# Performance work log

Hardware: AMD Instinct MI355X
Metric: run time of the kernel (lower is better)

## Reference

```python
import jax, jax.numpy as jnp
import numpy as np

NUM_HEADS = 4
CATEGORY_SIZE = 128
DIM = 192
B, N, M = 2, 65000, 64


def setup_inputs() -> dict:
    key = jax.random.key(0)
    k1, k2, k3, k4 = jax.random.split(key, 4)
    qkv = jax.random.normal(k1, (B, N, 3 * DIM), dtype=jnp.float32)
    sim = jax.random.normal(k2, (B, N, M), dtype=jnp.float32)
    proj_w = jax.random.normal(k3, (DIM, DIM), dtype=jnp.float32) * (1.0 / np.sqrt(DIM))
    proj_b = jax.random.normal(k4, (DIM,), dtype=jnp.float32) * 0.01
    logit_scale = jnp.log(10.0 * jnp.ones((1, 1), dtype=jnp.float32))
    return {"qkv": qkv, "sim": sim, "proj_w": proj_w, "proj_b": proj_b,
            "logit_scale": logit_scale, "x_size": 65000}


def reference(qkv, sim, proj_w, proj_b, logit_scale, x_size):
    b, n, c3 = qkv.shape
    c = c3 // 3
    h = NUM_HEADS
    gs = min(n, CATEGORY_SIZE)
    ng = (n + gs - 1) // gs
    pad_n = ng * gs - n

    # token -> category id, then sort tokens by category
    tk_id = jnp.argmax(sim, axis=-1)                      # (b, n) int
    sort_idx = jnp.argsort(tk_id, axis=-1)                # (b, n)
    inv_idx = jnp.argsort(sort_idx, axis=-1)              # inverse permutation

    shuffled = jnp.take_along_axis(qkv, sort_idx[..., None], axis=1)  # (b, n, 3c)
    if pad_n > 0:
        pad = jnp.flip(shuffled[:, n - pad_n:n, :], axis=1)
        shuffled = jnp.concatenate([shuffled, pad], axis=1)           # (b, n+pad_n, 3c)

    # (3, b, ng, h, gs, c/h)
    y = shuffled.reshape(b, ng, gs, 3, h, c // h).transpose(3, 0, 1, 4, 2, 5)
    q, k, v = y[0], y[1], y[2]

    scale = jnp.exp(jnp.minimum(logit_scale, jnp.log(jnp.asarray(100.0, dtype=qkv.dtype))))
    attn = jnp.einsum('bghqd,bghkd->bghqk', q, k) * scale  # (b, ng, h, gs, gs)
    attn = jax.nn.softmax(attn, axis=-1)
    out = jnp.einsum('bghqk,bghkd->bghqd', attn, v)        # (b, ng, h, gs, c/h)
    out = out.transpose(0, 1, 3, 2, 4).reshape(b, n + pad_n, c)[:, :n, :]

    # scatter back to original token order
    out = jnp.take_along_axis(out, inv_idx[..., None], axis=1)
    return out @ proj_w.T + proj_b
```

## Files before the change

kernel.cpp:

```cpp
#include <hip/hip_runtime.h>
#include <hip/hip_bf16.h>
#include <math.h>

#define BB 2
#define NN 65000
#define MM 64
#define DIM 192
#define NH 4
#define HD 48
#define GS 128
#define NG 508
#define SORT_TPB 256
#define NBLK 254

#define XROWS 65024
#define XTILES_B 1016

typedef __attribute__((ext_vector_type(8))) short bf16x8;
typedef __attribute__((ext_vector_type(8))) _Float16 f16x8;
typedef __attribute__((ext_vector_type(2))) __fp16 fp16x2;
typedef __attribute__((ext_vector_type(4))) float f32x4;
typedef __attribute__((ext_vector_type(16))) float f32x16;
typedef __attribute__((ext_vector_type(8))) unsigned short u16x8;

__device__ __forceinline__ unsigned short f2bf(float f) {
  __hip_bfloat16 h = __float2bfloat16(f);
  return *(unsigned short*)&h;
}
__device__ __forceinline__ unsigned int pkh(float lo, float hi) {
  fp16x2 t = __builtin_amdgcn_cvt_pkrtz(lo, hi);
  return *(unsigned int*)&t;
}
__device__ __forceinline__ f16x8 cvt8h(float4 a, float4 b) {
  f16x8 r;
  r[0] = (_Float16)a.x; r[1] = (_Float16)a.y; r[2] = (_Float16)a.z; r[3] = (_Float16)a.w;
  r[4] = (_Float16)b.x; r[5] = (_Float16)b.y; r[6] = (_Float16)b.z; r[7] = (_Float16)b.w;
  return r;
}
__device__ __forceinline__ void gload_lds16(const float* src, float* lds_dst) {
  __builtin_amdgcn_global_load_lds(
      (const __attribute__((address_space(1))) unsigned int*)src,
      (__attribute__((address_space(3))) unsigned int*)lds_dst, 16, 0, 0);
}

__global__ void k_argmax_hist(const float* __restrict__ sim, int* __restrict__ tk,
                              int* __restrict__ hist) {
  __shared__ int cnt[MM];
  const int b = blockIdx.y, blk = blockIdx.x;
  if (threadIdx.x < MM) cnt[threadIdx.x] = 0;
  __syncthreads();
  int t = blk * SORT_TPB + threadIdx.x;
  if (t < NN) {
    const float4* row = (const float4*)(sim + ((size_t)b * NN + t) * MM);
    float best = -INFINITY;
    int bi = 0;
#pragma unroll
    for (int j = 0; j < MM / 4; ++j) {
      float4 v = row[j];
      if (v.x > best) { best = v.x; bi = 4 * j + 0; }
      if (v.y > best) { best = v.y; bi = 4 * j + 1; }
      if (v.z > best) { best = v.z; bi = 4 * j + 2; }
      if (v.w > best) { best = v.w; bi = 4 * j + 3; }
    }
    tk[b * NN + t] = bi;
    atomicAdd(&cnt[bi], 1);
  }
  __syncthreads();
  if (threadIdx.x < MM)
    hist[(b * NBLK + blk) * MM + threadIdx.x] = cnt[threadIdx.x];
}

#define SEGS 16
#define SEGB 16
__global__ void k_scan(const int* __restrict__ hist, int* __restrict__ boff) {
  const int b = blockIdx.x;
  const int tid = threadIdx.x;
  const int seg = tid >> 6, bin = tid & 63;
  __shared__ int part[SEGS][MM];
  __shared__ int basev[MM];
  const int lo = seg * SEGB;
  const int hi = min(NBLK, lo + SEGB);
  int s = 0;
  for (int blk = lo; blk < hi; ++blk) s += hist[(b * NBLK + blk) * MM + bin];
  part[seg][bin] = s;
  __syncthreads();
  if (tid < 64) {
    int tot = 0;
#pragma unroll
    for (int s2 = 0; s2 < SEGS; ++s2) tot += part[s2][bin];
    int incl = tot;
#pragma unroll
    for (int d = 1; d < 64; d <<= 1) {
      int o = __shfl_up(incl, d);
      if (bin >= d) incl += o;
    }
    basev[bin] = incl - tot;
  }
  __syncthreads();
  int run = basev[bin];
  for (int s2 = 0; s2 < seg; ++s2) run += part[s2][bin];
  for (int blk = lo; blk < hi; ++blk) {
    int h = hist[(b * NBLK + blk) * MM + bin];
    boff[(b * NBLK + blk) * MM + bin] = run;
    run += h;
  }
}

__global__ void k_scatter(const int* __restrict__ tk, const int* __restrict__ boff,
                          int* __restrict__ sidx) {
  __shared__ int whist[4][MM];
  const int b = blockIdx.y, blk = blockIdx.x;
  const int tid = threadIdx.x;
  const int w = tid >> 6, lane = tid & 63;
  ((int*)whist)[tid] = 0;
  __syncthreads();
  int t = blk * SORT_TPB + tid;
  int bin = (t < NN) ? tk[b * NN + t] : -1;
  unsigned long long m = ~0ull;
#pragma unroll
  for (int bit = 0; bit < 6; ++bit) {
    unsigned long long bl = __ballot((bin >> bit) & 1);
    m &= ((bin >> bit) & 1) ? bl : ~bl;
  }
  int rank_w = __popcll(m & ((1ull << lane) - 1ull));
  if (bin >= 0 && rank_w == 0) whist[w][bin] = __popcll(m);
  __syncthreads();
  if (bin >= 0) {
    int rank = rank_w;
#pragma unroll
    for (int w2 = 0; w2 < 3; ++w2)
      if (w2 < w) rank += whist[w2][bin];
    int pos = boff[(b * NBLK + blk) * MM + bin] + rank;
    sidx[b * NN + pos] = t;
  }
}

__global__ __launch_bounds__(256) void k_attn_mfma(const float* __restrict__ qkv,
                                                   const int* __restrict__ sidx,
                                                   const float* __restrict__ logit_scale,
                                                   __hip_bfloat16* __restrict__ attn_out) {
  const int x = blockIdx.x;
  const int g = ((x >> 5) << 3) + (x & 7);
  const int hd = (x >> 3) & 3;
  const int b = blockIdx.z;
  if (g >= NG) return;

  __shared__ int stok[GS];
  __shared__ __align__(16) _Float16 akv[4 * 3 * 64 * 8];
  __shared__ __align__(16) _Float16 vfrag[2 * 8 * 64 * 8];

  const int tid = threadIdx.x;
  const int w = tid >> 6, l = tid & 63;
  const int hl = l >> 5, l31 = l & 31;

  if (tid < GS) {
    int s = g * GS + tid;
    int sp = (s < NN) ? s : (2 * NN - 1 - s);
    stok[tid] = sidx[b * NN + sp];
  }
  __syncthreads();

#pragma unroll
  for (int i = 0; i < 3; ++i) {
    int c = tid + 256 * i;
    int ts = c >> 6, cl = c & 63;
    int kvr = (ts / 3) * 32 + (cl & 31);
    int dbase = (ts % 3) * 16 + (cl >> 5) * 8;
    const float* src = qkv + (size_t)(b * NN + stok[kvr]) * (3 * DIM) + DIM + hd * HD + dbase;
    ((f16x8*)akv)[c] = cvt8h(((const float4*)src)[0], ((const float4*)src)[1]);
  }

#pragma unroll
  for (int i = 0; i < 4; ++i) {
    int c = tid + 256 * i;
    int ntks = c >> 6, cl = c & 63;
    int nt = ntks >> 3, ks = ntks & 7;
    int d = nt * 32 + (cl & 31);
    int kvb = ks * 16 + (cl >> 5) * 8;
    _Float16 tmp[8];
    if (d < HD) {
#pragma unroll
      for (int e = 0; e < 8; ++e)
        tmp[e] = (_Float16)qkv[(size_t)(b * NN + stok[kvb + e]) * (3 * DIM) + 2 * DIM + hd * HD + d];
    } else {
#pragma unroll
      for (int e = 0; e < 8; ++e) tmp[e] = (_Float16)0.f;
    }
    ((f16x8*)vfrag)[c] = *(f16x8*)tmp;
  }

  f16x8 qf[3];
  {
    const float* qsrc = qkv + (size_t)(b * NN + stok[w * 32 + l31]) * (3 * DIM) + hd * HD;
#pragma unroll
    for (int s = 0; s < 3; ++s) {
      const float4* p = (const float4*)(qsrc + s * 16 + hl * 8);
      qf[s] = cvt8h(p[0], p[1]);
    }
  }
  __syncthreads();

  f32x16 accS[4];
#pragma unroll
  for (int t = 0; t < 4; ++t)
#pragma unroll
    for (int r = 0; r < 16; ++r) accS[t][r] = 0.f;

#pragma unroll
  for (int t = 0; t < 4; ++t)
#pragma unroll
    for (int s = 0; s < 3; ++s) {
      f16x8 af = ((const f16x8*)akv)[(t * 3 + s) * 64 + l];
      accS[t] = __builtin_amdgcn_mfma_f32_32x32x16_f16(af, qf[s], accS[t], 0, 0, 0);
    }

  const float scale = expf(fminf(logit_scale[0], 4.6051701860f));
  float mx = -INFINITY;
#pragma unroll
  for (int t = 0; t < 4; ++t)
#pragma unroll
    for (int r = 0; r < 16; ++r) { accS[t][r] *= scale; mx = fmaxf(mx, accS[t][r]); }
  mx = fmaxf(mx, __shfl_xor(mx, 32));
  float sum = 0.f;
#pragma unroll
  for (int t = 0; t < 4; ++t)
#pragma unroll
    for (int r = 0; r < 16; ++r) { float p = __expf(accS[t][r] - mx); accS[t][r] = p; sum += p; }
  sum += __shfl_xor(sum, 32);
  const float inv = 1.f / sum;
#pragma unroll
  for (int t = 0; t < 4; ++t)
#pragma unroll
    for (int r = 0; r < 16; ++r) accS[t][r] *= inv;

  f32x16 accO[2];
#pragma unroll
  for (int nt = 0; nt < 2; ++nt)
#pragma unroll
    for (int r = 0; r < 16; ++r) accO[nt][r] = 0.f;

#pragma unroll
  for (int t = 0; t < 4; ++t) {
    union { unsigned int u[4]; f16x8 v; } fa, fb;
    {
      unsigned int a0 = pkh(accS[t][0], accS[t][1]);
      unsigned int a1 = pkh(accS[t][2], accS[t][3]);
      unsigned int b0 = pkh(accS[t][4], accS[t][5]);
      unsigned int b1 = pkh(accS[t][6], accS[t][7]);
      unsigned int sa0 = __shfl_xor(a0, 32), sa1 = __shfl_xor(a1, 32);
      unsigned int sb0 = __shfl_xor(b0, 32), sb1 = __shfl_xor(b1, 32);
      fa.u[0] = hl ? sb0 : a0; fa.u[1] = hl ? sb1 : a1;
      fa.u[2] = hl ? b0 : sa0; fa.u[3] = hl ? b1 : sa1;
    }
    {
      unsigned int a0 = pkh(accS[t][8], accS[t][9]);
      unsigned int a1 = pkh(accS[t][10], accS[t][11]);
      unsigned int b0 = pkh(accS[t][12], accS[t][13]);
      unsigned int b1 = pkh(accS[t][14], accS[t][15]);
      unsigned int sa0 = __shfl_xor(a0, 32), sa1 = __shfl_xor(a1, 32);
      unsigned int sb0 = __shfl_xor(b0, 32), sb1 = __shfl_xor(b1, 32);
      fb.u[0] = hl ? sb0 : a0; fb.u[1] = hl ? sb1 : a1;
      fb.u[2] = hl ? b0 : sa0; fb.u[3] = hl ? b1 : sa1;
    }
    accO[0] = __builtin_amdgcn_mfma_f32_32x32x16_f16(fa.v, ((const f16x8*)vfrag)[(0 * 8 + 2 * t) * 64 + l], accO[0], 0, 0, 0);
    accO[1] = __builtin_amdgcn_mfma_f32_32x32x16_f16(fa.v, ((const f16x8*)vfrag)[(1 * 8 + 2 * t) * 64 + l], accO[1], 0, 0, 0);
    accO[0] = __builtin_amdgcn_mfma_f32_32x32x16_f16(fb.v, ((const f16x8*)vfrag)[(0 * 8 + 2 * t + 1) * 64 + l], accO[0], 0, 0, 0);
    accO[1] = __builtin_amdgcn_mfma_f32_32x32x16_f16(fb.v, ((const f16x8*)vfrag)[(1 * 8 + 2 * t + 1) * 64 + l], accO[1], 0, 0, 0);
  }

#pragma unroll
  for (int r = 0; r < 16; ++r) {
    int rowl = w * 32 + (r & 3) + 8 * (r >> 2) + 4 * hl;
    int sg = g * GS + rowl;
    if (sg < NN) {
      size_t base = ((size_t)b * XROWS + sg) * DIM + hd * HD;
      attn_out[base + l31] = __float2bfloat16(accO[0][r]);
      if (l31 < 16) attn_out[base + 32 + l31] = __float2bfloat16(accO[1][r]);
    }
  }
}

__global__ void k_wpack(const float* __restrict__ W, unsigned short* __restrict__ wpack) {
  int idx = blockIdx.x * blockDim.x + threadIdx.x;
  if (idx >= 12 * 6 * 64) return;
  int lane = idx & 63;
  int kkjt = idx >> 6;
  int kk = kkjt % 6;
  int jt = kkjt / 6;
  int j = jt * 16 + (lane & 15);
  int k0 = kk * 32 + (lane >> 4) * 8;
  const float* src = W + (size_t)j * DIM + k0;
  unsigned short tmp[8];
#pragma unroll
  for (int e = 0; e < 8; ++e) tmp[e] = f2bf(src[e]);
  ((u16x8*)wpack)[idx] = *(const u16x8*)tmp;
}

__global__ __launch_bounds__(256) void k_proj_mfma(const unsigned short* __restrict__ xb,
                                                   const int* __restrict__ sidx,
                                                   const unsigned short* __restrict__ wpack,
                                                   const float* __restrict__ bias,
                                                   float* __restrict__ out) {
  __shared__ unsigned short wl[12 * 6 * 64 * 8];
  const int tid = threadIdx.x;

#pragma unroll
  for (int j = 0; j < 18; ++j) {
    int c = j * 256 + tid;
    gload_lds16((const float*)((const u16x8*)wpack + c), (float*)((u16x8*)wl + c));
  }

  const int wid = tid >> 6, lane = tid & 63;
  const int l15 = lane & 15, lk = lane >> 4;

  float bv[12];
#pragma unroll
  for (int jt = 0; jt < 12; ++jt) bv[jt] = bias[jt * 16 + l15];

  __syncthreads();

  for (int tile = blockIdx.x; tile < BB * XTILES_B; tile += gridDim.x) {
    const int b = tile / XTILES_B;
    const int r0 = (tile % XTILES_B) * 64 + wid * 16;
    f32x4 acc[12];
#pragma unroll
    for (int jt = 0; jt < 12; ++jt) { f32x4 t = {bv[jt], bv[jt], bv[jt], bv[jt]}; acc[jt] = t; }

    const unsigned short* xrow = xb + ((size_t)b * XROWS + r0 + l15) * DIM;
#pragma unroll
    for (int kk = 0; kk < 6; ++kk) {
      bf16x8 a = *(const bf16x8*)(xrow + kk * 32 + lk * 8);
#pragma unroll
      for (int jt = 0; jt < 12; ++jt) {
        bf16x8 bfr = *(const bf16x8*)(wl + ((jt * 6 + kk) * 64 + lane) * 8);
        acc[jt] = __builtin_amdgcn_mfma_f32_16x16x32_bf16(a, bfr, acc[jt], 0, 0, 0);
      }
    }

    const int rowb = r0 + lk * 4;
    int orow[4];
#pragma unroll
    for (int r = 0; r < 4; ++r)
      orow[r] = (rowb + r < NN) ? sidx[b * NN + rowb + r] : -1;

#pragma unroll
    for (int jt = 0; jt < 12; ++jt) {
#pragma unroll
      for (int r = 0; r < 4; ++r) {
        if (orow[r] >= 0)
          out[((size_t)b * NN + orow[r]) * DIM + jt * 16 + l15] = acc[jt][r];
      }
    }
  }
}

extern "C" void kernel_launch(void* const* d_in, const int* in_sizes, int n_in,
                              void* d_out, int out_size, void* d_ws, size_t ws_size,
                              hipStream_t stream) {
  const float* qkv = (const float*)d_in[0];
  const float* sim = (const float*)d_in[1];
  const float* proj_w = (const float*)d_in[2];
  const float* proj_b = (const float*)d_in[3];
  const float* logit_scale = (const float*)d_in[4];

  unsigned short* x_bf16 = (unsigned short*)d_ws;
  unsigned short* wpack = x_bf16 + (size_t)BB * XROWS * DIM;
  int* tk = (int*)(wpack + 12 * 6 * 64 * 8);
  int* hist = tk + (size_t)BB * NN;
  int* boff = hist + (size_t)BB * NBLK * MM;
  int* sidx = boff + (size_t)BB * NBLK * MM;

  k_argmax_hist<<<dim3(NBLK, BB), SORT_TPB, 0, stream>>>(sim, tk, hist);
  k_scan<<<BB, 1024, 0, stream>>>(hist, boff);
  k_scatter<<<dim3(NBLK, BB), SORT_TPB, 0, stream>>>(tk, boff, sidx);
  k_wpack<<<(12 * 6 * 64 + 255) / 256, 256, 0, stream>>>(proj_w, wpack);
  k_attn_mfma<<<dim3(2048, 1, BB), 256, 0, stream>>>(qkv, sidx, logit_scale,
                                                     (__hip_bfloat16*)x_bf16);
  k_proj_mfma<<<dim3(1016), 256, 0, stream>>>(x_bf16, sidx, wpack, proj_b, (float*)d_out);
}
```

Baseline: 161.5 us.

## Process all four heads of a group in one 1024-thread attention block

The attention kernel now launches one 1024-thread block per group and batch, with each 256-thread slice handling one head, instead of one 256-thread block per (group, head). The sorted-token index load into shared memory happens once per group rather than once per head, and the padded grid entries with early return are gone. Shared memory per block grows fourfold, and 1024-thread blocks with heavy MFMA register use may cap occupancy or constrain register allocation under the larger launch bound.

```diff
diff --git a/kernel.cpp b/kernel.cpp
--- a/kernel.cpp
+++ b/kernel.cpp
@@ -135,22 +135,21 @@
   }
 }
 
-__global__ __launch_bounds__(256) void k_attn_mfma(const float* __restrict__ qkv,
-                                                   const int* __restrict__ sidx,
-                                                   const float* __restrict__ logit_scale,
-                                                   __hip_bfloat16* __restrict__ attn_out) {
-  const int x = blockIdx.x;
-  const int g = ((x >> 5) << 3) + (x & 7);
-  const int hd = (x >> 3) & 3;
+__global__ __launch_bounds__(1024) void k_attn_mfma(const float* __restrict__ qkv,
+                                                    const int* __restrict__ sidx,
+                                                    const float* __restrict__ logit_scale,
+                                                    __hip_bfloat16* __restrict__ attn_out) {
+  const int g = blockIdx.x;
   const int b = blockIdx.z;
-  if (g >= NG) return;
 
   __shared__ int stok[GS];
-  __shared__ __align__(16) _Float16 akv[4 * 3 * 64 * 8];
-  __shared__ __align__(16) _Float16 vfrag[2 * 8 * 64 * 8];
+  __shared__ __align__(16) _Float16 akv[NH][4 * 3 * 64 * 8];
+  __shared__ __align__(16) _Float16 vfrag[NH][2 * 8 * 64 * 8];
 
   const int tid = threadIdx.x;
-  const int w = tid >> 6, l = tid & 63;
+  const int hd = tid >> 8;
+  const int t256 = tid & 255;
+  const int w = t256 >> 6, l = tid & 63;
   const int hl = l >> 5, l31 = l & 31;
 
   if (tid < GS) {
@@ -162,17 +161,17 @@
 
 #pragma unroll
   for (int i = 0; i < 3; ++i) {
-    int c = tid + 256 * i;
+    int c = t256 + 256 * i;
     int ts = c >> 6, cl = c & 63;
     int kvr = (ts / 3) * 32 + (cl & 31);
     int dbase = (ts % 3) * 16 + (cl >> 5) * 8;
     const float* src = qkv + (size_t)(b * NN + stok[kvr]) * (3 * DIM) + DIM + hd * HD + dbase;
-    ((f16x8*)akv)[c] = cvt8h(((const float4*)src)[0], ((const float4*)src)[1]);
+    ((f16x8*)akv[hd])[c] = cvt8h(((const float4*)src)[0], ((const float4*)src)[1]);
   }
 
 #pragma unroll
   for (int i = 0; i < 4; ++i) {
-    int c = tid + 256 * i;
+    int c = t256 + 256 * i;
     int ntks = c >> 6, cl = c & 63;
     int nt = ntks >> 3, ks = ntks & 7;
     int d = nt * 32 + (cl & 31);
@@ -186,7 +185,7 @@
 #pragma unroll
       for (int e = 0; e < 8; ++e) tmp[e] = (_Float16)0.f;
     }
-    ((f16x8*)vfrag)[c] = *(f16x8*)tmp;
+    ((f16x8*)vfrag[hd])[c] = *(f16x8*)tmp;
   }
 
   f16x8 qf[3];
@@ -210,7 +209,7 @@
   for (int t = 0; t < 4; ++t)
 #pragma unroll
     for (int s = 0; s < 3; ++s) {
-      f16x8 af = ((const f16x8*)akv)[(t * 3 + s) * 64 + l];
+      f16x8 af = ((const f16x8*)akv[hd])[(t * 3 + s) * 64 + l];
       accS[t] = __builtin_amdgcn_mfma_f32_32x32x16_f16(af, qf[s], accS[t], 0, 0, 0);
     }
 
@@ -262,10 +261,10 @@
       fb.u[0] = hl ? sb0 : a0; fb.u[1] = hl ? sb1 : a1;
       fb.u[2] = hl ? b0 : sa0; fb.u[3] = hl ? b1 : sa1;
     }
-    accO[0] = __builtin_amdgcn_mfma_f32_32x32x16_f16(fa.v, ((const f16x8*)vfrag)[(0 * 8 + 2 * t) * 64 + l], accO[0], 0, 0, 0);
-    accO[1] = __builtin_amdgcn_mfma_f32_32x32x16_f16(fa.v, ((const f16x8*)vfrag)[(1 * 8 + 2 * t) * 64 + l], accO[1], 0, 0, 0);
-    accO[0] = __builtin_amdgcn_mfma_f32_32x32x16_f16(fb.v, ((const f16x8*)vfrag)[(0 * 8 + 2 * t + 1) * 64 + l], accO[0], 0, 0, 0);
-    accO[1] = __builtin_amdgcn_mfma_f32_32x32x16_f16(fb.v, ((const f16x8*)vfrag)[(1 * 8 + 2 * t + 1) * 64 + l], accO[1], 0, 0, 0);
+    accO[0] = __builtin_amdgcn_mfma_f32_32x32x16_f16(fa.v, ((const f16x8*)vfrag[hd])[(0 * 8 + 2 * t) * 64 + l], accO[0], 0, 0, 0);
+    accO[1] = __builtin_amdgcn_mfma_f32_32x32x16_f16(fa.v, ((const f16x8*)vfrag[hd])[(1 * 8 + 2 * t) * 64 + l], accO[1], 0, 0, 0);
+    accO[0] = __builtin_amdgcn_mfma_f32_32x32x16_f16(fb.v, ((const f16x8*)vfrag[hd])[(0 * 8 + 2 * t + 1) * 64 + l], accO[0], 0, 0, 0);
+    accO[1] = __builtin_amdgcn_mfma_f32_32x32x16_f16(fb.v, ((const f16x8*)vfrag[hd])[(1 * 8 + 2 * t + 1) * 64 + l], accO[1], 0, 0, 0);
   }
 
 #pragma unroll
@@ -374,7 +373,7 @@
   k_scan<<<BB, 1024, 0, stream>>>(hist, boff);
   k_scatter<<<dim3(NBLK, BB), SORT_TPB, 0, stream>>>(tk, boff, sidx);
   k_wpack<<<(12 * 6 * 64 + 255) / 256, 256, 0, stream>>>(proj_w, wpack);
-  k_attn_mfma<<<dim3(2048, 1, BB), 256, 0, stream>>>(qkv, sidx, logit_scale,
-                                                     (__hip_bfloat16*)x_bf16);
+  k_attn_mfma<<<dim3(NG, 1, BB), 1024, 0, stream>>>(qkv, sidx, logit_scale,
+                                                    (__hip_bfloat16*)x_bf16);
   k_proj_mfma<<<dim3(1016), 256, 0, stream>>>(x_bf16, sidx, wpack, proj_b, (float*)d_out);
 }
```

After: 174.5 us. 1.08x slower.
